# Kernel optimization log

Hardware: AMD Instinct MI355X
Metric: run time of the kernel (lower is better)

Reference implementation:

```python
import jax, jax.numpy as jnp
import numpy as np

N_NODES = 65536
N_EDGES = 1048576
DIM = 64  # in_dim == out_dim == pooling kernel size


def setup_inputs() -> dict:
    key = jax.random.key(0)
    ks = jax.random.split(key, 6)
    s = 1.0 / np.sqrt(DIM)
    return {
        "x": jax.random.normal(ks[0], (N_NODES, DIM), dtype=jnp.float32),
        "edge_index": jax.random.randint(ks[1], (2, N_EDGES), 0, N_NODES, dtype=jnp.int32),
        "edge_weight": jax.random.uniform(ks[2], (N_EDGES,), dtype=jnp.float32),
        "W1": jax.random.normal(ks[3], (DIM, DIM), dtype=jnp.float32) * s,
        "b1": jnp.zeros((DIM,), dtype=jnp.float32),
        "W2": jax.random.normal(ks[4], (DIM, DIM), dtype=jnp.float32) * s,
        "b2": jnp.zeros((DIM,), dtype=jnp.float32),
    }


def gcn_conv(x, edge_index, edge_weight, W, b):
    """PyG GCNConv: symmetric-normalized aggregation with implicit self-loops (weight 1)."""
    n = x.shape[0]
    row, col = edge_index[0], edge_index[1]  # messages flow row -> col
    # degree includes self-loop weight 1
    deg = jnp.zeros((n,), dtype=x.dtype).at[col].add(edge_weight) + 1.0
    dinv = jnp.where(deg > 0, jax.lax.rsqrt(deg), 0.0)
    norm = dinv[row] * edge_weight * dinv[col]  # [E]
    h = x @ W  # linear transform first (no bias, bias added after aggregation)
    out = jnp.zeros_like(h).at[col].add(norm[:, None] * h[row])
    # self-loop message: norm = dinv[i]*1*dinv[i]
    out = out + h * (dinv * dinv)[:, None]
    return out + b


def reference(x, edge_index, edge_weight, W1, b1, W2, b2):
    h = gcn_conv(x, edge_index, edge_weight, W1, b1)
    h = gcn_conv(h, edge_index, edge_weight, W2, b2)  # [N, D]
    # AvgPool1d(kernel=D) over node axis of [1, D, N]: windows of D nodes, stride D
    n, d = h.shape
    m = n // d  # number of full windows
    pooled = h[: m * d].reshape(m, d, d).mean(axis=1)  # [M, D]
    return pooled.T  # squeeze -> [D, M]
```

## Files before the change

kernel.cpp:

```cpp
#include <hip/hip_runtime.h>

#define N_NODES 65536
#define N_EDGES 1048576
#define DIM 64
#define M_POOL (N_NODES / DIM)
#define NCOARSE 256
#define SEGCAP 5120
#define P3CHUNK 2048
#define P3BLOCKS (N_EDGES / P3CHUNK)
#define GEMM_BLOCKS 1024
#define FUSED_BLOCKS (GEMM_BLOCKS + P3BLOCKS)

typedef unsigned int u32;
typedef unsigned short u16;

__device__ __forceinline__ float bf2f(u32 hi16) {
    return __uint_as_float(hi16 << 16);
}
__device__ __forceinline__ u32 f2bf(float f) {
    u32 u = __float_as_uint(f);
    return (u + 0x7fffu + ((u >> 16) & 1u)) >> 16;
}

__device__ __forceinline__ void scan256_wave(int* arr, int* wsum, int t) {
    int s = 0;
    if (t < 256) {
        s = arr[t];
        const int lane = t & 63;
#pragma unroll
        for (int o = 1; o < 64; o <<= 1) {
            const int u = __shfl_up(s, o, 64);
            if (lane >= o) s += u;
        }
        if (lane == 63) wsum[t >> 6] = s;
    }
    __syncthreads();
    if (t < 256) {
        const int w = t >> 6;
        int add = 0;
#pragma unroll
        for (int k = 0; k < 4; ++k)
            if (k < w) add += wsum[k];
        arr[t] = s + add;
    }
    __syncthreads();
}


__global__ __launch_bounds__(256) void zero_cursor(int* __restrict__ cursor) {
    cursor[threadIdx.x] = 0;
}


__global__ __launch_bounds__(1024) void fused_gemm_p3(const float* __restrict__ x,
                                                      const float* __restrict__ W,
                                                      u16* __restrict__ hb,
                                                      const int* __restrict__ col,
                                                      const int* __restrict__ row,
                                                      const float* __restrict__ ew,
                                                      int* __restrict__ cursor,
                                                      int2* __restrict__ csr_tmp) {
    __shared__ __align__(16) char sm[33280];
    const int t = threadIdx.x;
    const int b = blockIdx.x;

    if ((b % 3) == 2) {
        int2* stg      = (int2*)sm;
        int*  gpA      = (int*)(sm + 16384);
        int*  h2       = (int*)(sm + 24576);
        int*  off      = (int*)(sm + 25600);
        int*  base_blk = (int*)(sm + 26624);
        int*  wsum     = (int*)(sm + 27648);
        const int e0 = (b / 3) * P3CHUNK + t * 2;

        if (t < NCOARSE) h2[t] = 0;
        __syncthreads();

        const int2 c2 = *(const int2*)&col[e0];
        const int2 r2 = *(const int2*)&row[e0];
        const float2 w2 = *(const float2*)&ew[e0];
        const int cc[2] = {c2.x >> 8, c2.y >> 8};

        atomicAdd(&h2[cc[0]], 1);
        atomicAdd(&h2[cc[1]], 1);
        __syncthreads();

        const int myc = (t < NCOARSE) ? h2[t] : 0;
        if (t < NCOARSE) off[t] = myc;
        __syncthreads();
        scan256_wave(off, wsum, t);
        if (t < NCOARSE) {
            off[t] -= myc;
            base_blk[t] = myc ? atomicAdd(&cursor[t], myc) : 0;
            h2[t] = 0;
        }
        __syncthreads();

        const int fi[2] = {c2.x & 255, c2.y & 255};
        const int rr[2] = {r2.x, r2.y};
        const float wv[2] = {w2.x, w2.y};
#pragma unroll
        for (int j = 0; j < 2; ++j) {
            const int c = cc[j];
            const int r = atomicAdd(&h2[c], 1);
            const int s = off[c] + r;
            const int bp = base_blk[c] + r;
            stg[s] = make_int2((rr[j] << 8) | fi[j], __float_as_int(wv[j]));
            gpA[s] = (bp < SEGCAP) ? (c * SEGCAP + bp) : -1;
        }
        __syncthreads();
        for (int i = t; i < P3CHUNK; i += 1024) {
            const int gp = gpA[i];
            if (gp >= 0) csr_tmp[gp] = stg[i];
        }
    } else {
        float* Ws = (float*)sm;
        float* Xs = (float*)(sm + 16384);
        const int row0 = (b - b / 3) * 64;
        for (int i = t; i < DIM * DIM; i += 1024) Ws[i] = W[i];
        for (int i = t; i < 64 * DIM; i += 1024)
            Xs[i] = x[(size_t)row0 * DIM + i];
        __syncthreads();
        const int j = t & 63;
        const int rs = t >> 6;
        for (int rrr = 0; rrr < 4; ++rrr) {
            const int r = rs * 4 + rrr;
            float acc = 0.f;
#pragma unroll
            for (int k = 0; k < DIM; ++k) acc += Xs[r * DIM + k] * Ws[k * DIM + j];
            hb[(size_t)(row0 + r) * DIM + j] = (u16)f2bf(acc);
        }
    }
}


__global__ __launch_bounds__(512) void p4_fine(const int* __restrict__ cursor,
                                               const int2* __restrict__ csr_tmp,
                                               u32* __restrict__ csr,
                                               int* __restrict__ rowptr,
                                               float* __restrict__ dinv,
                                               u16* __restrict__ hb) {
    __shared__ int2 A[SEGCAP];
    __shared__ u32 Bu[SEGCAP];
    __shared__ int fh[NCOARSE];
    __shared__ int off2[NCOARSE];
    __shared__ int cbase[NCOARSE];
    __shared__ float degw[NCOARSE];
    __shared__ float dvs[NCOARSE];
    __shared__ int wsum[4];
    const int t = threadIdx.x;
    const int c = blockIdx.x;
    const int segN = min(cursor[c], SEGCAP);

    if (t < NCOARSE) cbase[t] = min(cursor[t], SEGCAP);
    __syncthreads();
    scan256_wave(cbase, wsum, t);
    const int seg0_out = cbase[c] - segN;

    for (int i = t; i < segN; i += 512) A[i] = csr_tmp[c * SEGCAP + i];
    if (t < NCOARSE) { fh[t] = 0; degw[t] = 0.f; }
    __syncthreads();

    for (int i = t; i < segN; i += 512) {
        const int f = A[i].x & 255;
        atomicAdd(&fh[f], 1);
        atomicAdd(&degw[f], __int_as_float(A[i].y));
    }
    __syncthreads();

    if (t < NCOARSE) off2[t] = fh[t];
    __syncthreads();
    scan256_wave(off2, wsum, t);
    if (t < NCOARSE) {
        off2[t] -= fh[t];
        const float dv = rsqrtf(1.0f + degw[t]);
        dvs[t] = dv;
        dinv[c * 256 + t] = dv;
        rowptr[c * 256 + t] = seg0_out + off2[t];
        fh[t] = 0;
    }
    if (c == NCOARSE - 1 && t == 0) rowptr[N_NODES] = seg0_out + segN;
    __syncthreads();

    for (int idx = t; idx < 256 * 8; idx += 512) {
        const int nl = idx >> 3;
        const int part = idx & 7;
        const float dv = dvs[nl];
        const size_t p = (size_t)(c * 256 + nl) * DIM + part * 8;
        uint4 v = *(const uint4*)&hb[p];
        uint4 o;
        o.x = f2bf(dv * bf2f(v.x & 0xffff)) | (f2bf(dv * bf2f(v.x >> 16)) << 16);
        o.y = f2bf(dv * bf2f(v.y & 0xffff)) | (f2bf(dv * bf2f(v.y >> 16)) << 16);
        o.z = f2bf(dv * bf2f(v.z & 0xffff)) | (f2bf(dv * bf2f(v.z >> 16)) << 16);
        o.w = f2bf(dv * bf2f(v.w & 0xffff)) | (f2bf(dv * bf2f(v.w >> 16)) << 16);
        *(uint4*)&hb[p] = o;
    }

    for (int i = t; i < segN; i += 512) {
        const int f = A[i].x & 255;
        const int r = atomicAdd(&fh[f], 1);
        const float w = __int_as_float(A[i].y) * dvs[f];
        Bu[off2[f] + r] = (f2bf(w) << 16) | ((u32)(A[i].x >> 8) & 0xffffu);
    }
    __syncthreads();
    for (int i = t; i < segN; i += 512)
        csr[seg0_out + i] = Bu[i];
}


__global__ __launch_bounds__(256) void aggregate_l1(const int* __restrict__ rowptr,
                                                    const u32* __restrict__ csr,
                                                    const u16* __restrict__ hb2,
                                                    const float* __restrict__ dinv,
                                                    const float* __restrict__ bias,
                                                    u16* __restrict__ ob) {
    const int lane = threadIdx.x & 63;
    const int node = (blockIdx.x * 256 + threadIdx.x) >> 6;
    const int g = lane >> 3;
    const int q = lane & 7;
    const int start = rowptr[node];
    const int end = rowptr[node + 1];
    const float dv = dinv[node];

    float acc[8];
#pragma unroll
    for (int k = 0; k < 8; ++k) acc[k] = 0.f;

    for (int i = start; i < end; i += 16) {
        const int i0 = i + g;
        const int i1 = i + 8 + g;
        const u32 v0 = (i0 < end) ? csr[i0] : 0;
        const u32 v1 = (i1 < end) ? csr[i1] : 0;
        const float w0 = bf2f(v0 >> 16);
        const float w1 = bf2f(v1 >> 16);
        const uint4 B0 = *(const uint4*)&hb2[(size_t)(v0 & 0xffffu) * DIM + q * 8];
        const uint4 B1 = *(const uint4*)&hb2[(size_t)(v1 & 0xffffu) * DIM + q * 8];
        acc[0] += w0 * bf2f(B0.x & 0xffff) + w1 * bf2f(B1.x & 0xffff);
        acc[1] += w0 * bf2f(B0.x >> 16)    + w1 * bf2f(B1.x >> 16);
        acc[2] += w0 * bf2f(B0.y & 0xffff) + w1 * bf2f(B1.y & 0xffff);
        acc[3] += w0 * bf2f(B0.y >> 16)    + w1 * bf2f(B1.y >> 16);
        acc[4] += w0 * bf2f(B0.z & 0xffff) + w1 * bf2f(B1.z & 0xffff);
        acc[5] += w0 * bf2f(B0.z >> 16)    + w1 * bf2f(B1.z >> 16);
        acc[6] += w0 * bf2f(B0.w & 0xffff) + w1 * bf2f(B1.w & 0xffff);
        acc[7] += w0 * bf2f(B0.w >> 16)    + w1 * bf2f(B1.w >> 16);
    }
#pragma unroll
    for (int m = 8; m <= 32; m <<= 1) {
#pragma unroll
        for (int k = 0; k < 8; ++k) acc[k] += __shfl_xor(acc[k], m, 64);
    }
    if (lane < 8) {
        const uint4 S = *(const uint4*)&hb2[(size_t)node * DIM + q * 8];
        float r[8];
        r[0] = dv * (acc[0] + dv * bf2f(S.x & 0xffff) + bias[q * 8 + 0]);
        r[1] = dv * (acc[1] + dv * bf2f(S.x >> 16)    + bias[q * 8 + 1]);
        r[2] = dv * (acc[2] + dv * bf2f(S.y & 0xffff) + bias[q * 8 + 2]);
        r[3] = dv * (acc[3] + dv * bf2f(S.y >> 16)    + bias[q * 8 + 3]);
        r[4] = dv * (acc[4] + dv * bf2f(S.z & 0xffff) + bias[q * 8 + 4]);
        r[5] = dv * (acc[5] + dv * bf2f(S.z >> 16)    + bias[q * 8 + 5]);
        r[6] = dv * (acc[6] + dv * bf2f(S.w & 0xffff) + bias[q * 8 + 6]);
        r[7] = dv * (acc[7] + dv * bf2f(S.w >> 16)    + bias[q * 8 + 7]);
        uint4 o;
        o.x = f2bf(r[0]) | (f2bf(r[1]) << 16);
        o.y = f2bf(r[2]) | (f2bf(r[3]) << 16);
        o.z = f2bf(r[4]) | (f2bf(r[5]) << 16);
        o.w = f2bf(r[6]) | (f2bf(r[7]) << 16);
        *(uint4*)&ob[(size_t)node * DIM + q * 8] = o;
    }
}


__global__ __launch_bounds__(512) void agg2_pool_gemm(const int* __restrict__ rowptr,
                                                      const u32* __restrict__ csr,
                                                      const u16* __restrict__ hb,
                                                      const float* __restrict__ dinv,
                                                      const float* __restrict__ W2,
                                                      const float* __restrict__ b2,
                                                      float* __restrict__ out) {
    __shared__ float Ws[DIM * DIM];
    __shared__ float wacc[8][DIM];
    __shared__ float pooled[DIM];
    const int t = threadIdx.x;
    const int m = blockIdx.x;

    for (int i = t; i < DIM * DIM; i += 512) Ws[i] = W2[i];

    const int wave = t >> 6;
    const int lane = t & 63;
    const int g = lane >> 3;
    const int q = lane & 7;

    const int start = rowptr[m * 64];
    const int end = rowptr[m * 64 + 64];

    float acc[8];
#pragma unroll
    for (int k = 0; k < 8; ++k) acc[k] = 0.f;

    for (int i = start + wave * 32; i < end; i += 256) {
        const int i0 = i + g;
        const int i1 = i + 8 + g;
        const int i2 = i + 16 + g;
        const int i3 = i + 24 + g;
        const u32 v0 = (i0 < end) ? csr[i0] : 0;
        const u32 v1 = (i1 < end) ? csr[i1] : 0;
        const u32 v2 = (i2 < end) ? csr[i2] : 0;
        const u32 v3 = (i3 < end) ? csr[i3] : 0;
        const float w0 = bf2f(v0 >> 16);
        const float w1 = bf2f(v1 >> 16);
        const float w2 = bf2f(v2 >> 16);
        const float w3 = bf2f(v3 >> 16);
        const uint4 B0 = *(const uint4*)&hb[(size_t)(v0 & 0xffffu) * DIM + q * 8];
        const uint4 B1 = *(const uint4*)&hb[(size_t)(v1 & 0xffffu) * DIM + q * 8];
        const uint4 B2 = *(const uint4*)&hb[(size_t)(v2 & 0xffffu) * DIM + q * 8];
        const uint4 B3 = *(const uint4*)&hb[(size_t)(v3 & 0xffffu) * DIM + q * 8];
        acc[0] += w0 * bf2f(B0.x & 0xffff) + w1 * bf2f(B1.x & 0xffff)
                + w2 * bf2f(B2.x & 0xffff) + w3 * bf2f(B3.x & 0xffff);
        acc[1] += w0 * bf2f(B0.x >> 16)    + w1 * bf2f(B1.x >> 16)
                + w2 * bf2f(B2.x >> 16)    + w3 * bf2f(B3.x >> 16);
        acc[2] += w0 * bf2f(B0.y & 0xffff) + w1 * bf2f(B1.y & 0xffff)
                + w2 * bf2f(B2.y & 0xffff) + w3 * bf2f(B3.y & 0xffff);
        acc[3] += w0 * bf2f(B0.y >> 16)    + w1 * bf2f(B1.y >> 16)
                + w2 * bf2f(B2.y >> 16)    + w3 * bf2f(B3.y >> 16);
        acc[4] += w0 * bf2f(B0.z & 0xffff) + w1 * bf2f(B1.z & 0xffff)
                + w2 * bf2f(B2.z & 0xffff) + w3 * bf2f(B3.z & 0xffff);
        acc[5] += w0 * bf2f(B0.z >> 16)    + w1 * bf2f(B1.z >> 16)
                + w2 * bf2f(B2.z >> 16)    + w3 * bf2f(B3.z >> 16);
        acc[6] += w0 * bf2f(B0.w & 0xffff) + w1 * bf2f(B1.w & 0xffff)
                + w2 * bf2f(B2.w & 0xffff) + w3 * bf2f(B3.w & 0xffff);
        acc[7] += w0 * bf2f(B0.w >> 16)    + w1 * bf2f(B1.w >> 16)
                + w2 * bf2f(B2.w >> 16)    + w3 * bf2f(B3.w >> 16);
    }

    {
        const int node = m * 64 + wave * 8 + g;
        const float dv = dinv[node];
        const uint4 S = *(const uint4*)&hb[(size_t)node * DIM + q * 8];
        acc[0] += dv * bf2f(S.x & 0xffff);
        acc[1] += dv * bf2f(S.x >> 16);
        acc[2] += dv * bf2f(S.y & 0xffff);
        acc[3] += dv * bf2f(S.y >> 16);
        acc[4] += dv * bf2f(S.z & 0xffff);
        acc[5] += dv * bf2f(S.z >> 16);
        acc[6] += dv * bf2f(S.w & 0xffff);
        acc[7] += dv * bf2f(S.w >> 16);
    }

#pragma unroll
    for (int mm = 8; mm <= 32; mm <<= 1) {
#pragma unroll
        for (int k = 0; k < 8; ++k) acc[k] += __shfl_xor(acc[k], mm, 64);
    }
    if (lane < 8) {
#pragma unroll
        for (int k = 0; k < 8; ++k) wacc[wave][q * 8 + k] = acc[k];
    }
    __syncthreads();
    if (t < DIM) {
        float p = 0.f;
#pragma unroll
        for (int w = 0; w < 8; ++w) p += wacc[w][t];
        pooled[t] = p * (1.0f / DIM);
    }
    __syncthreads();
    if (t < DIM) {
        float o = b2[t];
#pragma unroll
        for (int k = 0; k < DIM; ++k) o += pooled[k] * Ws[k * DIM + t];
        out[(size_t)t * M_POOL + m] = o;
    }
}


extern "C" void kernel_launch(void* const* d_in, const int* in_sizes, int n_in,
                              void* d_out, int out_size, void* d_ws, size_t ws_size,
                              hipStream_t stream) {
    const float* x  = (const float*)d_in[0];
    const int*   ei = (const int*)d_in[1];
    const float* ew = (const float*)d_in[2];
    const float* W1 = (const float*)d_in[3];
    const float* b1 = (const float*)d_in[4];
    const float* W2 = (const float*)d_in[5];
    const float* b2 = (const float*)d_in[6];
    float* out = (float*)d_out;

    char* w = (char*)d_ws;
    int*   cursor = (int*)w;   w += 1024;
    int*   rowptr = (int*)w;   w += (size_t)(N_NODES + 16) * 4;
    float* dinv   = (float*)w; w += (size_t)N_NODES * 4;
    int2*  csrt   = (int2*)w;  w += (size_t)NCOARSE * SEGCAP * 8;
    u32*   csr    = (u32*)w;   w += (size_t)N_EDGES * 4;
    u16*   hbf    = (u16*)w;   w += (size_t)N_NODES * DIM * 2;
    u16*   h1bf   = (u16*)w;

    const int* row = ei;
    const int* col = ei + N_EDGES;

    zero_cursor<<<1, 256, 0, stream>>>(cursor);
    fused_gemm_p3<<<FUSED_BLOCKS, 1024, 0, stream>>>(x, W1, hbf, col, row, ew,
                                                     cursor, csrt);
    p4_fine<<<NCOARSE, 512, 0, stream>>>(cursor, csrt, csr, rowptr, dinv, hbf);

    aggregate_l1<<<N_NODES / 4, 256, 0, stream>>>(rowptr, csr, hbf, dinv, b1, h1bf);

    agg2_pool_gemm<<<M_POOL, 512, 0, stream>>>(rowptr, csr, h1bf, dinv, W2, b2, out);
}
```

Baseline: 123.6 us.

## Shrink fused GEMM/bucketing blocks and scatter bucketed edges directly

The fused GEMM plus edge-bucketing kernel moves from 1024-thread to 256-thread blocks, with each edge block handling 1024 edges (4 per thread) and each GEMM block 32 rows. The shared-memory staging of bucketed edges and the separate copy-out pass are removed, so each edge is written straight to its global segment slot after taking a local rank. The aim is lower shared-memory use, one fewer barrier, and more blocks resident at once. The cost is less coalesced global writes and twice as many cursor atomics, since there are twice as many edge blocks.

New measurement: 116.5 us. 1.06x faster.

```diff
diff --git a/kernel.cpp b/kernel.cpp
--- a/kernel.cpp
+++ b/kernel.cpp
@@ -6,9 +6,10 @@
 #define M_POOL (N_NODES / DIM)
 #define NCOARSE 256
 #define SEGCAP 5120
-#define P3CHUNK 2048
+#define P3CHUNK 1024
 #define P3BLOCKS (N_EDGES / P3CHUNK)
-#define GEMM_BLOCKS 1024
+#define GEMM_ROWS 32
+#define GEMM_BLOCKS (N_NODES / GEMM_ROWS)
 #define FUSED_BLOCKS (GEMM_BLOCKS + P3BLOCKS)
 
 typedef unsigned int u32;
@@ -52,79 +53,72 @@
 }
 
 
-__global__ __launch_bounds__(1024) void fused_gemm_p3(const float* __restrict__ x,
-                                                      const float* __restrict__ W,
-                                                      u16* __restrict__ hb,
-                                                      const int* __restrict__ col,
-                                                      const int* __restrict__ row,
-                                                      const float* __restrict__ ew,
-                                                      int* __restrict__ cursor,
-                                                      int2* __restrict__ csr_tmp) {
-    __shared__ __align__(16) char sm[33280];
+__global__ __launch_bounds__(256) void fused_gemm_p3(const float* __restrict__ x,
+                                                     const float* __restrict__ W,
+                                                     u16* __restrict__ hb,
+                                                     const int* __restrict__ col,
+                                                     const int* __restrict__ row,
+                                                     const float* __restrict__ ew,
+                                                     int* __restrict__ cursor,
+                                                     int2* __restrict__ csr_tmp) {
+    __shared__ __align__(16) char sm[24832];
     const int t = threadIdx.x;
     const int b = blockIdx.x;
 
     if ((b % 3) == 2) {
-        int2* stg      = (int2*)sm;
-        int*  gpA      = (int*)(sm + 16384);
-        int*  h2       = (int*)(sm + 24576);
-        int*  off      = (int*)(sm + 25600);
-        int*  base_blk = (int*)(sm + 26624);
-        int*  wsum     = (int*)(sm + 27648);
-        const int e0 = (b / 3) * P3CHUNK + t * 2;
-
-        if (t < NCOARSE) h2[t] = 0;
+        int* h2       = (int*)sm;
+        int* off      = (int*)(sm + 1024);
+        int* base_blk = (int*)(sm + 2048);
+        int* wsum     = (int*)(sm + 3072);
+        const int e0 = (b / 3) * P3CHUNK + t * 4;
+
+        h2[t] = 0;
         __syncthreads();
 
-        const int2 c2 = *(const int2*)&col[e0];
-        const int2 r2 = *(const int2*)&row[e0];
-        const float2 w2 = *(const float2*)&ew[e0];
-        const int cc[2] = {c2.x >> 8, c2.y >> 8};
+        const int4 c4 = *(const int4*)&col[e0];
+        const int4 r4 = *(const int4*)&row[e0];
+        const float4 w4 = *(const float4*)&ew[e0];
+        const int cc[4] = {c4.x >> 8, c4.y >> 8, c4.z >> 8, c4.w >> 8};
 
         atomicAdd(&h2[cc[0]], 1);
         atomicAdd(&h2[cc[1]], 1);
+        atomicAdd(&h2[cc[2]], 1);
+        atomicAdd(&h2[cc[3]], 1);
         __syncthreads();
 
-        const int myc = (t < NCOARSE) ? h2[t] : 0;
-        if (t < NCOARSE) off[t] = myc;
+        const int myc = h2[t];
+        off[t] = myc;
         __syncthreads();
         scan256_wave(off, wsum, t);
-        if (t < NCOARSE) {
-            off[t] -= myc;
-            base_blk[t] = myc ? atomicAdd(&cursor[t], myc) : 0;
-            h2[t] = 0;
-        }
+        off[t] -= myc;
+        base_blk[t] = myc ? atomicAdd(&cursor[t], myc) : 0;
+        h2[t] = 0;
         __syncthreads();
 
-        const int fi[2] = {c2.x & 255, c2.y & 255};
-        const int rr[2] = {r2.x, r2.y};
-        const float wv[2] = {w2.x, w2.y};
-#pragma unroll
-        for (int j = 0; j < 2; ++j) {
+        const int fi[4] = {c4.x & 255, c4.y & 255, c4.z & 255, c4.w & 255};
+        const int rr[4] = {r4.x, r4.y, r4.z, r4.w};
+        const float wv[4] = {w4.x, w4.y, w4.z, w4.w};
+#pragma unroll
+        for (int j = 0; j < 4; ++j) {
             const int c = cc[j];
             const int r = atomicAdd(&h2[c], 1);
-            const int s = off[c] + r;
             const int bp = base_blk[c] + r;
-            stg[s] = make_int2((rr[j] << 8) | fi[j], __float_as_int(wv[j]));
-            gpA[s] = (bp < SEGCAP) ? (c * SEGCAP + bp) : -1;
-        }
-        __syncthreads();
-        for (int i = t; i < P3CHUNK; i += 1024) {
-            const int gp = gpA[i];
-            if (gp >= 0) csr_tmp[gp] = stg[i];
+            if (bp < SEGCAP)
+                csr_tmp[c * SEGCAP + bp] =
+                    make_int2((rr[j] << 8) | fi[j], __float_as_int(wv[j]));
         }
     } else {
         float* Ws = (float*)sm;
         float* Xs = (float*)(sm + 16384);
-        const int row0 = (b - b / 3) * 64;
-        for (int i = t; i < DIM * DIM; i += 1024) Ws[i] = W[i];
-        for (int i = t; i < 64 * DIM; i += 1024)
+        const int row0 = (b - b / 3) * GEMM_ROWS;
+        for (int i = t; i < DIM * DIM; i += 256) Ws[i] = W[i];
+        for (int i = t; i < GEMM_ROWS * DIM; i += 256)
             Xs[i] = x[(size_t)row0 * DIM + i];
         __syncthreads();
         const int j = t & 63;
         const int rs = t >> 6;
-        for (int rrr = 0; rrr < 4; ++rrr) {
-            const int r = rs * 4 + rrr;
+        for (int rrr = 0; rrr < 8; ++rrr) {
+            const int r = rs * 8 + rrr;
             float acc = 0.f;
 #pragma unroll
             for (int k = 0; k < DIM; ++k) acc += Xs[r * DIM + k] * Ws[k * DIM + j];
@@ -397,8 +391,8 @@
     const int* col = ei + N_EDGES;
 
     zero_cursor<<<1, 256, 0, stream>>>(cursor);
-    fused_gemm_p3<<<FUSED_BLOCKS, 1024, 0, stream>>>(x, W1, hbf, col, row, ew,
-                                                     cursor, csrt);
+    fused_gemm_p3<<<FUSED_BLOCKS, 256, 0, stream>>>(x, W1, hbf, col, row, ew,
+                                                    cursor, csrt);
     p4_fine<<<NCOARSE, 512, 0, stream>>>(cursor, csrt, csr, rowptr, dinv, hbf);
 
     aggregate_l1<<<N_NODES / 4, 256, 0, stream>>>(rowptr, csr, hbf, dinv, b1, h1bf);
```
